# Kernel tuning notes

Measured on AMD Instinct MI355X. Metric: run time of the kernel, lower is better.

Reference implementation:

```python
import jax, jax.numpy as jnp
import numpy as np
from jax.scipy.linalg import expm

D_MODEL, D_STATE, BATCH, SEQ_LEN = 1024, 256, 8, 2048


def setup_inputs() -> dict:
    key = jax.random.key(0)
    k0, k1, k2, k3 = jax.random.split(key, 4)
    x = jax.random.normal(k0, (BATCH, SEQ_LEN, D_MODEL), dtype=jnp.float32)
    A = jax.random.normal(k1, (D_STATE, D_STATE), dtype=jnp.float32) * 0.01
    B = jax.random.normal(k2, (D_MODEL, D_STATE), dtype=jnp.float32) * 0.01
    C = jax.random.normal(k3, (D_STATE, D_MODEL), dtype=jnp.float32) * 0.01
    D = jnp.ones((D_MODEL,), dtype=jnp.float32)
    h0 = jnp.zeros((BATCH, D_STATE), dtype=jnp.float32)
    return {"x": x, "A": A, "B": B, "C": C, "D": D, "h0": h0}


def reference(x, A, B, C, D, h0):
    # Discretized transition: matrix exponential of A * dt (dt = 0.1)
    A_d = expm(A * 0.1)  # (n, n)
    # Input projection for all timesteps at once: u_t = x_t @ B
    u = jnp.einsum('bsd,dn->bsn', x, B)  # (b, s, n)

    def step(h, u_t):
        # h_t = h_{t-1} @ A_d + x_t @ B  (matches torch bmm order: row-vec times matrix)
        h = h @ A_d + u_t  # (b, n)
        return h, h

    _, hs = jax.lax.scan(step, h0, jnp.swapaxes(u, 0, 1))  # hs: (s, b, n)
    hs = jnp.swapaxes(hs, 0, 1)  # (b, s, n)
    # y_t = h_t @ C + x_t * D
    y = jnp.einsum('bsn,nd->bsd', hs, C) + x * D
    return y
```

## Files before the change

kernel.cpp:

```cpp
#include <hip/hip_runtime.h>

typedef float f4v __attribute__((ext_vector_type(4)));
typedef short s8v __attribute__((ext_vector_type(8)));

__device__ __forceinline__ unsigned short f2bf(float x){
  union { float f; unsigned u; } v; v.f = x;
  unsigned r = v.u + 0x7fffu + ((v.u >> 16) & 1u);
  return (unsigned short)(r >> 16);
}
__device__ __forceinline__ float bf2f(unsigned short b){
  union { unsigned u; float f; } v; v.u = ((unsigned)b) << 16;
  return v.f;
}
__device__ __forceinline__ void split8(const float* __restrict__ p, s8v& h, s8v& l){
  float4 v0 = *reinterpret_cast<const float4*>(p);
  float4 v1 = *reinterpret_cast<const float4*>(p + 4);
  float a[8] = {v0.x, v0.y, v0.z, v0.w, v1.x, v1.y, v1.z, v1.w};
#pragma unroll
  for (int j = 0; j < 8; ++j) {
    unsigned short hi = f2bf(a[j]);
    h[j] = (short)hi;
    l[j] = (short)f2bf(a[j] - bf2f(hi));
  }
}
__device__ __forceinline__ void zero8(s8v& v){
#pragma unroll
  for (int j = 0; j < 8; ++j) v[j] = 0;
}

__global__ void k_prep(const float* __restrict__ A, const float* __restrict__ B,
                       const float* __restrict__ C,
                       float* __restrict__ Mt, float* __restrict__ Tp0,
                       unsigned short* __restrict__ Bt, unsigned short* __restrict__ Ct){
  int i = blockIdx.x * 256 + threadIdx.x;
  const int tot = 65536 + 262144 + 262144;
  for (; i < tot; i += gridDim.x * 256) {
    if (i < 65536) {
      int r = i >> 8, c = i & 255;
      float m = 0.1f * A[c * 256 + r];
      Mt[i] = m;
      Tp0[i] = m * 0.25f + (r == c ? 1.0f : 0.0f);
    } else if (i < 65536 + 262144) {
      int j = i - 65536;
      int n = j >> 10, k = j & 1023;
      Bt[j] = f2bf(B[k * 256 + n]);
    } else {
      int j = i - 65536 - 262144;
      int col = j >> 8, n = j & 255;
      Ct[j] = f2bf(C[n * 1024 + col]);
    }
  }
}

__global__ __launch_bounds__(256) void k_taylor(const float* __restrict__ Mt,
    const float* __restrict__ Bsrc, float* __restrict__ Odst,
    unsigned short* __restrict__ QSh, unsigned short* __restrict__ QSl,
    unsigned short* __restrict__ Et, float alpha, int fin){
  __shared__ unsigned short Bh[64][40], Bl[64][40];
  int tid = threadIdx.x, lane = tid & 63, w = tid >> 6;
  int wr = w >> 1, wc = w & 1, l15 = lane & 15, quad = lane >> 4, q8 = quad * 8;
  int bid = blockIdx.x;
  int m0 = (bid >> 2) * 64, n0 = (bid & 3) * 64;
  f4v acc[2][2] = {};
  for (int kt = 0; kt < 256; kt += 32) {
    __syncthreads();
    {
      int col = tid & 63, kk0 = (tid >> 6) * 8;
#pragma unroll
      for (int j = 0; j < 8; ++j) {
        float v = Bsrc[(kt + kk0 + j) * 256 + n0 + col];
        unsigned short hi = f2bf(v);
        Bh[col][kk0 + j] = hi;
        Bl[col][kk0 + j] = f2bf(v - bf2f(hi));
      }
    }
    __syncthreads();
#pragma unroll
    for (int aq = 0; aq < 2; ++aq) {
      s8v ah, al;
      split8(&Mt[(m0 + wr * 32 + aq * 16 + l15) * 256 + kt + q8], ah, al);
#pragma unroll
      for (int bq = 0; bq < 2; ++bq) {
        s8v bh = *reinterpret_cast<const s8v*>(&Bh[wc * 32 + bq * 16 + l15][q8]);
        s8v bl = *reinterpret_cast<const s8v*>(&Bl[wc * 32 + bq * 16 + l15][q8]);
        acc[aq][bq] = __builtin_amdgcn_mfma_f32_16x16x32_bf16(ah, bh, acc[aq][bq], 0, 0, 0);
        acc[aq][bq] = __builtin_amdgcn_mfma_f32_16x16x32_bf16(ah, bl, acc[aq][bq], 0, 0, 0);
        acc[aq][bq] = __builtin_amdgcn_mfma_f32_16x16x32_bf16(al, bh, acc[aq][bq], 0, 0, 0);
      }
    }
  }
#pragma unroll
  for (int aq = 0; aq < 2; ++aq)
#pragma unroll
    for (int bq = 0; bq < 2; ++bq)
#pragma unroll
      for (int r = 0; r < 4; ++r) {
        int gm = m0 + wr * 32 + aq * 16 + quad * 4 + r;
        int gn = n0 + wc * 32 + bq * 16 + l15;
        float raw = alpha * acc[aq][bq][r];
        float v = raw + (gm == gn ? 1.0f : 0.0f);
        if (!fin) {
          Odst[gm * 256 + gn] = v;
        } else {
          unsigned short hi = f2bf(v);
          QSh[gm * 256 + gn] = hi;
          QSl[gm * 256 + gn] = f2bf(v - bf2f(hi));
          Et[gm * 256 + gn] = f2bf(raw);
        }
      }
}

__global__ __launch_bounds__(256) void k_power(unsigned short* __restrict__ QSh,
    unsigned short* __restrict__ QSl, int d){
  __shared__ unsigned short Bh[64][40], Bl[64][40];
  int tid = threadIdx.x, lane = tid & 63, w = tid >> 6;
  int wr = w >> 1, wc = w & 1, l15 = lane & 15, quad = lane >> 4, q8 = quad * 8;
  int bid = blockIdx.x;
  int mt = bid >> 2, nt = bid & 3;
  int m0 = mt * 64, n0 = nt * 64;
  int bro = (d - 1) * 256;
  f4v acc[2][2] = {};
  for (int kt = 0; kt < 256; kt += 32) {
    __syncthreads();
    {
      int col = tid & 63, kk0 = (tid >> 6) * 8;
#pragma unroll
      for (int j = 0; j < 8; ++j) {
        int k = kt + kk0 + j;
        Bh[col][kk0 + j] = QSh[(bro + k) * 256 + n0 + col];
        Bl[col][kk0 + j] = QSl[(bro + k) * 256 + n0 + col];
      }
    }
    __syncthreads();
#pragma unroll
    for (int aq = 0; aq < 2; ++aq) {
      s8v ah = *reinterpret_cast<const s8v*>(&QSh[(m0 + wr * 32 + aq * 16 + l15) * 256 + kt + q8]);
      s8v al = *reinterpret_cast<const s8v*>(&QSl[(m0 + wr * 32 + aq * 16 + l15) * 256 + kt + q8]);
#pragma unroll
      for (int bq = 0; bq < 2; ++bq) {
        s8v bh = *reinterpret_cast<const s8v*>(&Bh[wc * 32 + bq * 16 + l15][q8]);
        s8v bl = *reinterpret_cast<const s8v*>(&Bl[wc * 32 + bq * 16 + l15][q8]);
        acc[aq][bq] = __builtin_amdgcn_mfma_f32_16x16x32_bf16(ah, bh, acc[aq][bq], 0, 0, 0);
        acc[aq][bq] = __builtin_amdgcn_mfma_f32_16x16x32_bf16(ah, bl, acc[aq][bq], 0, 0, 0);
        acc[aq][bq] = __builtin_amdgcn_mfma_f32_16x16x32_bf16(al, bh, acc[aq][bq], 0, 0, 0);
      }
    }
  }
#pragma unroll
  for (int aq = 0; aq < 2; ++aq)
#pragma unroll
    for (int bq = 0; bq < 2; ++bq)
#pragma unroll
      for (int r = 0; r < 4; ++r) {
        int gm = m0 + wr * 32 + aq * 16 + quad * 4 + r;
        int gn = n0 + wc * 32 + bq * 16 + l15;
        float v = acc[aq][bq][r];
        unsigned short hi = f2bf(v);
        QSh[(d * 256 + gm) * 256 + gn] = hi;
        QSl[(d * 256 + gm) * 256 + gn] = f2bf(v - bf2f(hi));
      }
}

__global__ __launch_bounds__(256) void k_gemm_u(const float* __restrict__ x,
                                                const unsigned short* __restrict__ Bt,
                                                unsigned short* __restrict__ u){
  __shared__ unsigned short Atile[128][40];
  __shared__ unsigned short Btile[128][40];
  int tid = threadIdx.x;
  int m0 = blockIdx.x * 128, n0 = blockIdx.y * 128;
  int w = tid >> 6, lane = tid & 63;
  int wr = w >> 1, wc = w & 1;
  int l15 = lane & 15, quad = lane >> 4;
  int q8 = quad * 8;
  f4v acc[4][4] = {};
  for (int kt = 0; kt < 1024; kt += 32) {
    __syncthreads();
#pragma unroll
    for (int q = 0; q < 4; ++q) {
      int id = q * 256 + tid;
      int row = id >> 3, c4 = id & 7;
      float4 vv = *reinterpret_cast<const float4*>(&x[(m0 + row) * 1024 + kt + c4 * 4]);
      ushort4 hv;
      hv.x = f2bf(vv.x); hv.y = f2bf(vv.y); hv.z = f2bf(vv.z); hv.w = f2bf(vv.w);
      *reinterpret_cast<ushort4*>(&Atile[row][c4 * 4]) = hv;
    }
#pragma unroll
    for (int q = 0; q < 2; ++q) {
      int id = q * 256 + tid;
      int row = id >> 2, c8 = id & 3;
      uint4 vv = *reinterpret_cast<const uint4*>(&Bt[(n0 + row) * 1024 + kt + c8 * 8]);
      *reinterpret_cast<uint4*>(&Btile[row][c8 * 8]) = vv;
    }
    __syncthreads();
    s8v af[4], bf[4];
#pragma unroll
    for (int aq = 0; aq < 4; ++aq)
      af[aq] = *reinterpret_cast<const s8v*>(&Atile[wr * 64 + aq * 16 + l15][q8]);
#pragma unroll
    for (int bq = 0; bq < 4; ++bq)
      bf[bq] = *reinterpret_cast<const s8v*>(&Btile[wc * 64 + bq * 16 + l15][q8]);
#pragma unroll
    for (int aq = 0; aq < 4; ++aq)
#pragma unroll
      for (int bq = 0; bq < 4; ++bq)
        acc[aq][bq] = __builtin_amdgcn_mfma_f32_16x16x32_bf16(af[aq], bf[bq], acc[aq][bq], 0, 0, 0);
  }
#pragma unroll
  for (int aq = 0; aq < 4; ++aq)
#pragma unroll
    for (int bq = 0; bq < 4; ++bq)
#pragma unroll
      for (int r = 0; r < 4; ++r) {
        int gm = m0 + wr * 64 + aq * 16 + quad * 4 + r;
        int gn = n0 + wc * 64 + bq * 16 + l15;
        u[gm * 256 + gn] = f2bf(acc[aq][bq][r]);
      }
}

__global__ __launch_bounds__(256, 1) void k_phase1(const unsigned short* __restrict__ u,
                                                   const unsigned short* __restrict__ Et,
                                                   unsigned short* __restrict__ hs,
                                                   float* __restrict__ g0,
                                                   const float* __restrict__ h0){
  __shared__ unsigned short hbuf[2][16][264];
  int tid = threadIdx.x, w = tid >> 6, lane = tid & 63;
  int l15 = lane & 15, quad = lane >> 4;
  int U0 = blockIdx.x * 16;
  s8v e[4][8];
#pragma unroll
  for (int ct = 0; ct < 4; ++ct) {
    int col = w * 64 + ct * 16 + l15;
#pragma unroll
    for (int kt = 0; kt < 8; ++kt)
      e[ct][kt] = *reinterpret_cast<const s8v*>(&Et[col * 256 + kt * 32 + quad * 8]);
  }
  int rowbase[4];
#pragma unroll
  for (int r = 0; r < 4; ++r) {
    int g = U0 + quad * 4 + r;
    rowbase[r] = ((g >> 7) * 2048 + (g & 127) * 16) * 256;
  }
  for (int i = tid; i < 16 * 264; i += 256) hbuf[0][0][i] = 0;
  if (blockIdx.x == 0)
    for (int i = tid; i < 2048; i += 256) g0[i] = h0[i];
  f4v acc[4] = {};
  float uv[4][4];
#pragma unroll
  for (int r = 0; r < 4; ++r)
#pragma unroll
    for (int ct = 0; ct < 4; ++ct)
      uv[r][ct] = bf2f(u[rowbase[r] + w * 64 + ct * 16 + l15]);
  __syncthreads();
  int cur = 0;
  for (int t = 0; t < 16; ++t) {
    s8v af[8];
#pragma unroll
    for (int kt = 0; kt < 8; ++kt)
      af[kt] = *reinterpret_cast<const s8v*>(&hbuf[cur][l15][kt * 32 + quad * 8]);
    float uvn[4][4];
    if (t < 15)
#pragma unroll
      for (int r = 0; r < 4; ++r)
#pragma unroll
        for (int ct = 0; ct < 4; ++ct)
          uvn[r][ct] = bf2f(u[rowbase[r] + (t + 1) * 256 + w * 64 + ct * 16 + l15]);
#pragma unroll
    for (int kt = 0; kt < 8; ++kt)
#pragma unroll
      for (int ct = 0; ct < 4; ++ct)
        acc[ct] = __builtin_amdgcn_mfma_f32_16x16x32_bf16(af[kt], e[ct][kt], acc[ct], 0, 0, 0);
    int nxt = cur ^ 1;
#pragma unroll
    for (int ct = 0; ct < 4; ++ct)
#pragma unroll
      for (int r = 0; r < 4; ++r) {
        acc[ct][r] += uv[r][ct];
        hbuf[nxt][quad * 4 + r][w * 64 + ct * 16 + l15] = f2bf(acc[ct][r]);
      }
    __syncthreads();
    int ul = w * 4 + quad, seg = l15;
    uint4 d0 = *reinterpret_cast<const uint4*>(&hbuf[nxt][ul][seg * 16]);
    uint4 d1 = *reinterpret_cast<const uint4*>(&hbuf[nxt][ul][seg * 16 + 8]);
    int g = U0 + ul;
    int hrow = ((g >> 7) * 2048 + (g & 127) * 16 + t) * 256;
    *reinterpret_cast<uint4*>(&hs[hrow + seg * 16]) = d0;
    *reinterpret_cast<uint4*>(&hs[hrow + seg * 16 + 8]) = d1;
    if (t < 15)
#pragma unroll
      for (int r = 0; r < 4; ++r)
#pragma unroll
        for (int ct = 0; ct < 4; ++ct)
          uv[r][ct] = uvn[r][ct];
    cur = nxt;
  }
#pragma unroll
  for (int ct = 0; ct < 4; ++ct)
#pragma unroll
    for (int r = 0; r < 4; ++r) {
      int g = U0 + quad * 4 + r;
      int k = g & 127, b = g >> 7;
      if (k < 127)
        g0[((k + 1) * 8 + b) * 256 + w * 64 + ct * 16 + l15] = acc[ct][r];
    }
}

__global__ __launch_bounds__(256) void k_scanround(const float* __restrict__ gi,
    float* __restrict__ go,
    const unsigned short* __restrict__ cSh, const unsigned short* __restrict__ cSl,
    unsigned short* __restrict__ dh, unsigned short* __restrict__ dl,
    int rs, int dosq){
  __shared__ unsigned short Bh[64][40], Bl[64][40];
  int tid = threadIdx.x, lane = tid & 63, w = tid >> 6;
  int wr = w >> 1, wc = w & 1, l15 = lane & 15, quad = lane >> 4, q8 = quad * 8;
  int bid = blockIdx.x;
  if (bid < 64) {
    int mt = bid >> 2, nt = bid & 3;
    int m0 = mt * 64, n0 = nt * 64;
    f4v acc[2][2];
#pragma unroll
    for (int aq = 0; aq < 2; ++aq)
#pragma unroll
      for (int bq = 0; bq < 2; ++bq)
#pragma unroll
        for (int r = 0; r < 4; ++r)
          acc[aq][bq][r] = gi[(m0 + wr * 32 + aq * 16 + quad * 4 + r) * 256 +
                              n0 + wc * 32 + bq * 16 + l15];
    for (int kt = 0; kt < 256; kt += 32) {
      s8v ah[2], al[2];
#pragma unroll
      for (int aq = 0; aq < 2; ++aq) {
        int ar = m0 + wr * 32 + aq * 16 + l15 - rs;
        if (ar >= 0) split8(&gi[ar * 256 + kt + q8], ah[aq], al[aq]);
        else { zero8(ah[aq]); zero8(al[aq]); }
      }
#pragma unroll
      for (int bq = 0; bq < 2; ++bq) {
        int bc = n0 + wc * 32 + bq * 16 + l15;
        s8v bh = *reinterpret_cast<const s8v*>(&cSh[bc * 256 + kt + q8]);
        s8v bl = *reinterpret_cast<const s8v*>(&cSl[bc * 256 + kt + q8]);
#pragma unroll
        for (int aq = 0; aq < 2; ++aq) {
          acc[aq][bq] = __builtin_amdgcn_mfma_f32_16x16x32_bf16(ah[aq], bh, acc[aq][bq], 0, 0, 0);
          acc[aq][bq] = __builtin_amdgcn_mfma_f32_16x16x32_bf16(ah[aq], bl, acc[aq][bq], 0, 0, 0);
          acc[aq][bq] = __builtin_amdgcn_mfma_f32_16x16x32_bf16(al[aq], bh, acc[aq][bq], 0, 0, 0);
        }
      }
    }
#pragma unroll
    for (int aq = 0; aq < 2; ++aq)
#pragma unroll
      for (int bq = 0; bq < 2; ++bq)
#pragma unroll
        for (int r = 0; r < 4; ++r)
          go[(m0 + wr * 32 + aq * 16 + quad * 4 + r) * 256 +
             n0 + wc * 32 + bq * 16 + l15] = acc[aq][bq][r];
  } else if (dosq) {
    int t = bid - 64;
    int m0 = (t >> 2) * 64, n0 = (t & 3) * 64;
    f4v acc[2][2] = {};
    for (int kt = 0; kt < 256; kt += 32) {
      __syncthreads();
      {
        int col = tid & 63, kk0 = (tid >> 6) * 8;
#pragma unroll
        for (int j = 0; j < 8; ++j) {
          int k = kt + kk0 + j;
          Bh[col][kk0 + j] = cSh[k * 256 + n0 + col];
          Bl[col][kk0 + j] = cSl[k * 256 + n0 + col];
        }
      }
      __syncthreads();
#pragma unroll
      for (int aq = 0; aq < 2; ++aq) {
        s8v ah = *reinterpret_cast<const s8v*>(&cSh[(m0 + wr * 32 + aq * 16 + l15) * 256 + kt + q8]);
        s8v al = *reinterpret_cast<const s8v*>(&cSl[(m0 + wr * 32 + aq * 16 + l15) * 256 + kt + q8]);
#pragma unroll
        for (int bq = 0; bq < 2; ++bq) {
          s8v bh = *reinterpret_cast<const s8v*>(&Bh[wc * 32 + bq * 16 + l15][q8]);
          s8v bl = *reinterpret_cast<const s8v*>(&Bl[wc * 32 + bq * 16 + l15][q8]);
          acc[aq][bq] = __builtin_amdgcn_mfma_f32_16x16x32_bf16(ah, bh, acc[aq][bq], 0, 0, 0);
          acc[aq][bq] = __builtin_amdgcn_mfma_f32_16x16x32_bf16(ah, bl, acc[aq][bq], 0, 0, 0);
          acc[aq][bq] = __builtin_amdgcn_mfma_f32_16x16x32_bf16(al, bh, acc[aq][bq], 0, 0, 0);
        }
      }
    }
#pragma unroll
    for (int aq = 0; aq < 2; ++aq)
#pragma unroll
      for (int bq = 0; bq < 2; ++bq)
#pragma unroll
        for (int r = 0; r < 4; ++r) {
          int gm = m0 + wr * 32 + aq * 16 + quad * 4 + r;
          int gn = n0 + wc * 32 + bq * 16 + l15;
          float v = acc[aq][bq][r];
          unsigned short hi = f2bf(v);
          dh[gm * 256 + gn] = hi;
          dl[gm * 256 + gn] = f2bf(v - bf2f(hi));
        }
  }
}

__global__ __launch_bounds__(256) void k_carryexp(const float* __restrict__ g,
    const unsigned short* __restrict__ QSh, const unsigned short* __restrict__ QSl,
    unsigned short* __restrict__ hs){
  int tid = threadIdx.x, lane = tid & 63, w = tid >> 6;
  int wr = w >> 1, wc = w & 1, l15 = lane & 15, quad = lane >> 4, q8 = quad * 8;
  for (int t = blockIdx.x; t < 1024; t += 256) {
    int mt = t >> 6, nt = t & 63;
    int m0 = mt * 64, n0 = nt * 64;
    f4v acc[2][2] = {};
    for (int kt = 0; kt < 256; kt += 32) {
      s8v ah[2], al[2];
#pragma unroll
      for (int aq = 0; aq < 2; ++aq)
        split8(&g[(m0 + wr * 32 + aq * 16 + l15) * 256 + kt + q8], ah[aq], al[aq]);
#pragma unroll
      for (int bq = 0; bq < 2; ++bq) {
        int bc = n0 + wc * 32 + bq * 16 + l15;
        s8v bh = *reinterpret_cast<const s8v*>(&QSh[bc * 256 + kt + q8]);
        s8v bl = *reinterpret_cast<const s8v*>(&QSl[bc * 256 + kt + q8]);
#pragma unroll
        for (int aq = 0; aq < 2; ++aq) {
          acc[aq][bq] = __builtin_amdgcn_mfma_f32_16x16x32_bf16(ah[aq], bh, acc[aq][bq], 0, 0, 0);
          acc[aq][bq] = __builtin_amdgcn_mfma_f32_16x16x32_bf16(ah[aq], bl, acc[aq][bq], 0, 0, 0);
          acc[aq][bq] = __builtin_amdgcn_mfma_f32_16x16x32_bf16(al[aq], bh, acc[aq][bq], 0, 0, 0);
        }
      }
    }
#pragma unroll
    for (int aq = 0; aq < 2; ++aq)
#pragma unroll
      for (int bq = 0; bq < 2; ++bq)
#pragma unroll
        for (int r = 0; r < 4; ++r) {
          int gm = m0 + wr * 32 + aq * 16 + quad * 4 + r;
          int gn = n0 + wc * 32 + bq * 16 + l15;
          int k = gm >> 3, b = gm & 7, t0 = gn >> 8, nn = gn & 255;
          int idx = (b * 2048 + k * 16 + t0) * 256 + nn;
          hs[idx] = f2bf(bf2f(hs[idx]) + acc[aq][bq][r]);
        }
  }
}

__global__ __launch_bounds__(256) void k_gemm_y(const unsigned short* __restrict__ hs,
                                                const unsigned short* __restrict__ Ct,
                                                const float* __restrict__ x,
                                                const float* __restrict__ D,
                                                float* __restrict__ y){
  __shared__ unsigned short Atile[128][40];
  __shared__ unsigned short Btile[128][40];
  int tid = threadIdx.x;
  int m0 = blockIdx.x * 128, n0 = blockIdx.y * 128;
  int w = tid >> 6, lane = tid & 63;
  int wr = w >> 1, wc = w & 1;
  int l15 = lane & 15, quad = lane >> 4;
  int q8 = quad * 8;
  f4v acc[4][4] = {};
  for (int kt = 0; kt < 256; kt += 32) {
    __syncthreads();
#pragma unroll
    for (int q = 0; q < 2; ++q) {
      int id = q * 256 + tid;
      int row = id >> 2, c8 = id & 3;
      uint4 av = *reinterpret_cast<const uint4*>(&hs[(m0 + row) * 256 + kt + c8 * 8]);
      *reinterpret_cast<uint4*>(&Atile[row][c8 * 8]) = av;
      uint4 bv = *reinterpret_cast<const uint4*>(&Ct[(n0 + row) * 256 + kt + c8 * 8]);
      *reinterpret_cast<uint4*>(&Btile[row][c8 * 8]) = bv;
    }
    __syncthreads();
    s8v af[4], bf[4];
#pragma unroll
    for (int aq = 0; aq < 4; ++aq)
      af[aq] = *reinterpret_cast<const s8v*>(&Atile[wr * 64 + aq * 16 + l15][q8]);
#pragma unroll
    for (int bq = 0; bq < 4; ++bq)
      bf[bq] = *reinterpret_cast<const s8v*>(&Btile[wc * 64 + bq * 16 + l15][q8]);
#pragma unroll
    for (int aq = 0; aq < 4; ++aq)
#pragma unroll
      for (int bq = 0; bq < 4; ++bq)
        acc[aq][bq] = __builtin_amdgcn_mfma_f32_16x16x32_bf16(af[aq], bf[bq], acc[aq][bq], 0, 0, 0);
  }
#pragma unroll
  for (int bq = 0; bq < 4; ++bq) {
    int gn = n0 + wc * 64 + bq * 16 + l15;
    float dv = D[gn];
#pragma unroll
    for (int aq = 0; aq < 4; ++aq)
#pragma unroll
      for (int r = 0; r < 4; ++r) {
        int gm = m0 + wr * 64 + aq * 16 + quad * 4 + r;
        y[gm * 1024 + gn] = acc[aq][bq][r] + x[gm * 1024 + gn] * dv;
      }
  }
}

extern "C" void kernel_launch(void* const* d_in, const int* in_sizes, int n_in,
                              void* d_out, int out_size, void* d_ws, size_t ws_size,
                              hipStream_t stream) {
  (void)in_sizes; (void)n_in; (void)out_size; (void)ws_size;
  const float* x  = (const float*)d_in[0];
  const float* A  = (const float*)d_in[1];
  const float* B  = (const float*)d_in[2];
  const float* C  = (const float*)d_in[3];
  const float* D  = (const float*)d_in[4];
  const float* h0 = (const float*)d_in[5];
  float* y = (float*)d_out;

  char* ws = (char*)d_ws;
  size_t off = 0;
  auto alloc = [&](size_t bytes) { void* p = ws + off; off += (bytes + 255) & ~(size_t)255; return p; };
  float* Mt  = (float*)alloc(262144);
  float* Tp0 = (float*)alloc(262144);
  float* Tp1 = (float*)alloc(262144);
  unsigned short* QSh = (unsigned short*)alloc(2097152);
  unsigned short* QSl = (unsigned short*)alloc(2097152);
  unsigned short* Et  = (unsigned short*)alloc(131072);
  unsigned short* Sh0 = (unsigned short*)alloc(131072);
  unsigned short* Sl0 = (unsigned short*)alloc(131072);
  unsigned short* Sh1 = (unsigned short*)alloc(131072);
  unsigned short* Sl1 = (unsigned short*)alloc(131072);
  float* g0 = (float*)alloc(1048576);
  float* g1 = (float*)alloc(1048576);
  unsigned short* Bt = (unsigned short*)alloc(524288);
  unsigned short* Ct = (unsigned short*)alloc(524288);
  unsigned short* u  = (unsigned short*)alloc(8388608);
  unsigned short* hs = (unsigned short*)alloc(8388608);

  k_prep<<<2304, 256, 0, stream>>>(A, B, C, Mt, Tp0, Bt, Ct);

  k_taylor<<<16, 256, 0, stream>>>(Mt, Tp0, Tp1, QSh, QSl, Et, 1.0f / 3.0f, 0);
  k_taylor<<<16, 256, 0, stream>>>(Mt, Tp1, Tp0, QSh, QSl, Et, 0.5f, 0);
  k_taylor<<<16, 256, 0, stream>>>(Mt, Tp0, Tp1, QSh, QSl, Et, 1.0f, 1);

  for (int d = 1; d <= 8; d <<= 1)
    k_power<<<d * 16, 256, 0, stream>>>(QSh, QSl, d);

  k_gemm_u<<<dim3(128, 2), 256, 0, stream>>>(x, Bt, u);
  k_phase1<<<64, 256, 0, stream>>>(u, Et, hs, g0, h0);

  {
    const unsigned short* cSh = QSh + 15 * 65536;
    const unsigned short* cSl = QSl + 15 * 65536;
    float* gi = g0;
    float* go = g1;
    for (int rd = 0; rd < 7; ++rd) {
      int rs = 8 << rd;
      int dosq = (rd < 6) ? 1 : 0;
      unsigned short* dh = (rd & 1) ? Sh1 : Sh0;
      unsigned short* dl = (rd & 1) ? Sl1 : Sl0;
      k_scanround<<<dosq ? 80 : 64, 256, 0, stream>>>(gi, go, cSh, cSl, dh, dl, rs, dosq);
      if (dosq) {
        cSh = dh; cSl = dl;
        float* tg = gi; gi = go; go = tg;
      }
    }
  }

  k_carryexp<<<256, 256, 0, stream>>>(g1, QSh, QSl, hs);
  k_gemm_y<<<dim3(128, 8), 256, 0, stream>>>(hs, Ct, x, D, y);
}
```

Baseline: 448.2 us.

## Swap MFMA operand roles for vectorized epilogues and drop LDS staging in GEMMs

In the u, y and carry GEMMs, the MFMA operands are swapped so each lane's four accumulator values lie along the output's contiguous dimension. This lets the epilogues use 4-wide vector stores and loads (ushort4/float4) instead of scalar strided ones. The u and y GEMMs also drop shared-memory tiling and barriers, loading fragments straight from global memory into registers. This removes the LDS round-trips and syncs but loses data reuse across warps, so global and cache traffic may rise.

```diff
diff --git a/kernel.cpp b/kernel.cpp
--- a/kernel.cpp
+++ b/kernel.cpp
@@ -164,57 +164,49 @@
 __global__ __launch_bounds__(256) void k_gemm_u(const float* __restrict__ x,
                                                 const unsigned short* __restrict__ Bt,
                                                 unsigned short* __restrict__ u){
-  __shared__ unsigned short Atile[128][40];
-  __shared__ unsigned short Btile[128][40];
   int tid = threadIdx.x;
   int m0 = blockIdx.x * 128, n0 = blockIdx.y * 128;
   int w = tid >> 6, lane = tid & 63;
-  int wr = w >> 1, wc = w & 1;
-  int l15 = lane & 15, quad = lane >> 4;
-  int q8 = quad * 8;
+  int wm = w & 1, wn = w >> 1;
+  int l15 = lane & 15, quad = lane >> 4, q8 = quad * 8;
   f4v acc[4][4] = {};
+  const unsigned short* bbase = Bt + (n0 + wn * 64 + l15) * 1024;
+  const float* xbase = x + (size_t)(m0 + wm * 64 + l15) * 1024;
   for (int kt = 0; kt < 1024; kt += 32) {
-    __syncthreads();
-#pragma unroll
-    for (int q = 0; q < 4; ++q) {
-      int id = q * 256 + tid;
-      int row = id >> 3, c4 = id & 7;
-      float4 vv = *reinterpret_cast<const float4*>(&x[(m0 + row) * 1024 + kt + c4 * 4]);
+    s8v a[4], b[4];
+#pragma unroll
+    for (int nq = 0; nq < 4; ++nq)
+      a[nq] = *reinterpret_cast<const s8v*>(bbase + nq * 16 * 1024 + kt + q8);
+#pragma unroll
+    for (int mq = 0; mq < 4; ++mq) {
+      const float* p = xbase + mq * 16 * 1024 + kt + q8;
+      float4 v0 = *reinterpret_cast<const float4*>(p);
+      float4 v1 = *reinterpret_cast<const float4*>(p + 4);
+      s8v t;
+      t[0] = (short)f2bf(v0.x); t[1] = (short)f2bf(v0.y);
+      t[2] = (short)f2bf(v0.z); t[3] = (short)f2bf(v0.w);
+      t[4] = (short)f2bf(v1.x); t[5] = (short)f2bf(v1.y);
+      t[6] = (short)f2bf(v1.z); t[7] = (short)f2bf(v1.w);
+      b[mq] = t;
+    }
+#pragma unroll
+    for (int nq = 0; nq < 4; ++nq)
+#pragma unroll
+      for (int mq = 0; mq < 4; ++mq)
+        acc[nq][mq] = __builtin_amdgcn_mfma_f32_16x16x32_bf16(a[nq], b[mq], acc[nq][mq], 0, 0, 0);
+  }
+#pragma unroll
+  for (int nq = 0; nq < 4; ++nq) {
+    int nb = n0 + wn * 64 + nq * 16 + quad * 4;
+#pragma unroll
+    for (int mq = 0; mq < 4; ++mq) {
+      int m = m0 + wm * 64 + mq * 16 + l15;
       ushort4 hv;
-      hv.x = f2bf(vv.x); hv.y = f2bf(vv.y); hv.z = f2bf(vv.z); hv.w = f2bf(vv.w);
-      *reinterpret_cast<ushort4*>(&Atile[row][c4 * 4]) = hv;
-    }
-#pragma unroll
-    for (int q = 0; q < 2; ++q) {
-      int id = q * 256 + tid;
-      int row = id >> 2, c8 = id & 3;
-      uint4 vv = *reinterpret_cast<const uint4*>(&Bt[(n0 + row) * 1024 + kt + c8 * 8]);
-      *reinterpret_cast<uint4*>(&Btile[row][c8 * 8]) = vv;
-    }
-    __syncthreads();
-    s8v af[4], bf[4];
-#pragma unroll
-    for (int aq = 0; aq < 4; ++aq)
-      af[aq] = *reinterpret_cast<const s8v*>(&Atile[wr * 64 + aq * 16 + l15][q8]);
-#pragma unroll
-    for (int bq = 0; bq < 4; ++bq)
-      bf[bq] = *reinterpret_cast<const s8v*>(&Btile[wc * 64 + bq * 16 + l15][q8]);
-#pragma unroll
-    for (int aq = 0; aq < 4; ++aq)
-#pragma unroll
-      for (int bq = 0; bq < 4; ++bq)
-        acc[aq][bq] = __builtin_amdgcn_mfma_f32_16x16x32_bf16(af[aq], bf[bq], acc[aq][bq], 0, 0, 0);
-  }
-#pragma unroll
-  for (int aq = 0; aq < 4; ++aq)
-#pragma unroll
-    for (int bq = 0; bq < 4; ++bq)
-#pragma unroll
-      for (int r = 0; r < 4; ++r) {
-        int gm = m0 + wr * 64 + aq * 16 + quad * 4 + r;
-        int gn = n0 + wc * 64 + bq * 16 + l15;
-        u[gm * 256 + gn] = f2bf(acc[aq][bq][r]);
-      }
+      hv.x = f2bf(acc[nq][mq][0]); hv.y = f2bf(acc[nq][mq][1]);
+      hv.z = f2bf(acc[nq][mq][2]); hv.w = f2bf(acc[nq][mq][3]);
+      *reinterpret_cast<ushort4*>(&u[m * 256 + nb]) = hv;
+    }
+  }
 }
 
 __global__ __launch_bounds__(256, 1) void k_phase1(const unsigned short* __restrict__ u,
@@ -404,41 +396,47 @@
     const unsigned short* __restrict__ QSh, const unsigned short* __restrict__ QSl,
     unsigned short* __restrict__ hs){
   int tid = threadIdx.x, lane = tid & 63, w = tid >> 6;
-  int wr = w >> 1, wc = w & 1, l15 = lane & 15, quad = lane >> 4, q8 = quad * 8;
+  int wm = w & 1, wn = w >> 1, l15 = lane & 15, quad = lane >> 4, q8 = quad * 8;
   for (int t = blockIdx.x; t < 1024; t += 256) {
     int mt = t >> 6, nt = t & 63;
     int m0 = mt * 64, n0 = nt * 64;
     f4v acc[2][2] = {};
     for (int kt = 0; kt < 256; kt += 32) {
-      s8v ah[2], al[2];
-#pragma unroll
-      for (int aq = 0; aq < 2; ++aq)
-        split8(&g[(m0 + wr * 32 + aq * 16 + l15) * 256 + kt + q8], ah[aq], al[aq]);
-#pragma unroll
-      for (int bq = 0; bq < 2; ++bq) {
-        int bc = n0 + wc * 32 + bq * 16 + l15;
-        s8v bh = *reinterpret_cast<const s8v*>(&QSh[bc * 256 + kt + q8]);
-        s8v bl = *reinterpret_cast<const s8v*>(&QSl[bc * 256 + kt + q8]);
-#pragma unroll
-        for (int aq = 0; aq < 2; ++aq) {
-          acc[aq][bq] = __builtin_amdgcn_mfma_f32_16x16x32_bf16(ah[aq], bh, acc[aq][bq], 0, 0, 0);
-          acc[aq][bq] = __builtin_amdgcn_mfma_f32_16x16x32_bf16(ah[aq], bl, acc[aq][bq], 0, 0, 0);
-          acc[aq][bq] = __builtin_amdgcn_mfma_f32_16x16x32_bf16(al[aq], bh, acc[aq][bq], 0, 0, 0);
+      s8v bh[2], bl[2];
+#pragma unroll
+      for (int mq = 0; mq < 2; ++mq)
+        split8(&g[(m0 + wm * 32 + mq * 16 + l15) * 256 + kt + q8], bh[mq], bl[mq]);
+#pragma unroll
+      for (int nq = 0; nq < 2; ++nq) {
+        int pc = n0 + wn * 32 + nq * 16 + l15;
+        s8v ah = *reinterpret_cast<const s8v*>(&QSh[pc * 256 + kt + q8]);
+        s8v al = *reinterpret_cast<const s8v*>(&QSl[pc * 256 + kt + q8]);
+#pragma unroll
+        for (int mq = 0; mq < 2; ++mq) {
+          acc[nq][mq] = __builtin_amdgcn_mfma_f32_16x16x32_bf16(ah, bh[mq], acc[nq][mq], 0, 0, 0);
+          acc[nq][mq] = __builtin_amdgcn_mfma_f32_16x16x32_bf16(ah, bl[mq], acc[nq][mq], 0, 0, 0);
+          acc[nq][mq] = __builtin_amdgcn_mfma_f32_16x16x32_bf16(al, bh[mq], acc[nq][mq], 0, 0, 0);
         }
       }
     }
 #pragma unroll
-    for (int aq = 0; aq < 2; ++aq)
-#pragma unroll
-      for (int bq = 0; bq < 2; ++bq)
-#pragma unroll
-        for (int r = 0; r < 4; ++r) {
-          int gm = m0 + wr * 32 + aq * 16 + quad * 4 + r;
-          int gn = n0 + wc * 32 + bq * 16 + l15;
-          int k = gm >> 3, b = gm & 7, t0 = gn >> 8, nn = gn & 255;
-          int idx = (b * 2048 + k * 16 + t0) * 256 + nn;
-          hs[idx] = f2bf(bf2f(hs[idx]) + acc[aq][bq][r]);
-        }
+    for (int nq = 0; nq < 2; ++nq) {
+      int gn = n0 + wn * 32 + nq * 16 + quad * 4;
+      int t0 = gn >> 8, nn = gn & 255;
+#pragma unroll
+      for (int mq = 0; mq < 2; ++mq) {
+        int gm = m0 + wm * 32 + mq * 16 + l15;
+        int k = gm >> 3, b = gm & 7;
+        int idx = (b * 2048 + k * 16 + t0) * 256 + nn;
+        ushort4 hv = *reinterpret_cast<const ushort4*>(&hs[idx]);
+        ushort4 ov;
+        ov.x = f2bf(bf2f(hv.x) + acc[nq][mq][0]);
+        ov.y = f2bf(bf2f(hv.y) + acc[nq][mq][1]);
+        ov.z = f2bf(bf2f(hv.z) + acc[nq][mq][2]);
+        ov.w = f2bf(bf2f(hv.w) + acc[nq][mq][3]);
+        *reinterpret_cast<ushort4*>(&hs[idx]) = ov;
+      }
+    }
   }
 }
 
@@ -447,51 +445,43 @@
                                                 const float* __restrict__ x,
                                                 const float* __restrict__ D,
                                                 float* __restrict__ y){
-  __shared__ unsigned short Atile[128][40];
-  __shared__ unsigned short Btile[128][40];
   int tid = threadIdx.x;
   int m0 = blockIdx.x * 128, n0 = blockIdx.y * 128;
   int w = tid >> 6, lane = tid & 63;
-  int wr = w >> 1, wc = w & 1;
-  int l15 = lane & 15, quad = lane >> 4;
-  int q8 = quad * 8;
+  int wm = w & 1, wn = w >> 1;
+  int l15 = lane & 15, quad = lane >> 4, q8 = quad * 8;
   f4v acc[4][4] = {};
+  const unsigned short* cbase = Ct + (n0 + wn * 64 + l15) * 256;
+  const unsigned short* hbase = hs + (size_t)(m0 + wm * 64 + l15) * 256;
   for (int kt = 0; kt < 256; kt += 32) {
-    __syncthreads();
-#pragma unroll
-    for (int q = 0; q < 2; ++q) {
-      int id = q * 256 + tid;
-      int row = id >> 2, c8 = id & 3;
-      uint4 av = *reinterpret_cast<const uint4*>(&hs[(m0 + row) * 256 + kt + c8 * 8]);
-      *reinterpret_cast<uint4*>(&Atile[row][c8 * 8]) = av;
-      uint4 bv = *reinterpret_cast<const uint4*>(&Ct[(n0 + row) * 256 + kt + c8 * 8]);
-      *reinterpret_cast<uint4*>(&Btile[row][c8 * 8]) = bv;
-    }
-    __syncthreads();
-    s8v af[4], bf[4];
-#pragma unroll
-    for (int aq = 0; aq < 4; ++aq)
-      af[aq] = *reinterpret_cast<const s8v*>(&Atile[wr * 64 + aq * 16 + l15][q8]);
-#pragma unroll
-    for (int bq = 0; bq < 4; ++bq)
-      bf[bq] = *reinterpret_cast<const s8v*>(&Btile[wc * 64 + bq * 16 + l15][q8]);
-#pragma unroll
-    for (int aq = 0; aq < 4; ++aq)
-#pragma unroll
-      for (int bq = 0; bq < 4; ++bq)
-        acc[aq][bq] = __builtin_amdgcn_mfma_f32_16x16x32_bf16(af[aq], bf[bq], acc[aq][bq], 0, 0, 0);
-  }
-#pragma unroll
-  for (int bq = 0; bq < 4; ++bq) {
-    int gn = n0 + wc * 64 + bq * 16 + l15;
-    float dv = D[gn];
-#pragma unroll
-    for (int aq = 0; aq < 4; ++aq)
-#pragma unroll
-      for (int r = 0; r < 4; ++r) {
-        int gm = m0 + wr * 64 + aq * 16 + quad * 4 + r;
-        y[gm * 1024 + gn] = acc[aq][bq][r] + x[gm * 1024 + gn] * dv;
-      }
+    s8v a[4], b[4];
+#pragma unroll
+    for (int nq = 0; nq < 4; ++nq)
+      a[nq] = *reinterpret_cast<const s8v*>(cbase + nq * 16 * 256 + kt + q8);
+#pragma unroll
+    for (int mq = 0; mq < 4; ++mq)
+      b[mq] = *reinterpret_cast<const s8v*>(hbase + mq * 16 * 256 + kt + q8);
+#pragma unroll
+    for (int nq = 0; nq < 4; ++nq)
+#pragma unroll
+      for (int mq = 0; mq < 4; ++mq)
+        acc[nq][mq] = __builtin_amdgcn_mfma_f32_16x16x32_bf16(a[nq], b[mq], acc[nq][mq], 0, 0, 0);
+  }
+#pragma unroll
+  for (int nq = 0; nq < 4; ++nq) {
+    int nb = n0 + wn * 64 + nq * 16 + quad * 4;
+    float4 dv = *reinterpret_cast<const float4*>(&D[nb]);
+#pragma unroll
+    for (int mq = 0; mq < 4; ++mq) {
+      int m = m0 + wm * 64 + mq * 16 + l15;
+      float4 xv = *reinterpret_cast<const float4*>(&x[(size_t)m * 1024 + nb]);
+      float4 ov;
+      ov.x = acc[nq][mq][0] + xv.x * dv.x;
+      ov.y = acc[nq][mq][1] + xv.y * dv.y;
+      ov.z = acc[nq][mq][2] + xv.z * dv.z;
+      ov.w = acc[nq][mq][3] + xv.w * dv.w;
+      *reinterpret_cast<float4*>(&y[(size_t)m * 1024 + nb]) = ov;
+    }
   }
 }
 
```

After: 447.7 us. Within noise of the previous version (-0.1%).
